# Kernel tuning notes

Hardware: AMD Instinct MI355X
Metric: run time of the kernel (lower is better)

The kernel has to match this reference:

```python
import jax, jax.numpy as jnp
import numpy as np

B = 512
D_MODEL = 512
D_STATE = 128
D_CONV = 2
EXPAND = 2
D_INNER = EXPAND * D_MODEL          # 1024
DT_RANK = (D_MODEL + 15) // 16      # 32 (mamba default 'auto')
HIDDEN = 256


def setup_inputs() -> dict:
    key = jax.random.key(0)
    ks = jax.random.split(key, 12)
    s = 0.02
    f32 = jnp.float32
    inp = {
        "x": jax.random.normal(ks[0], (B, D_MODEL), f32),
        # Mamba params (torch Linear weight layout: [out, in])
        "in_proj_w": jax.random.normal(ks[1], (2 * D_INNER, D_MODEL), f32) * s,
        "conv_w": jax.random.normal(ks[2], (D_INNER, D_CONV), f32) * s,  # depthwise kernel
        "conv_b": jnp.zeros((D_INNER,), f32),
        "x_proj_w": jax.random.normal(ks[3], (DT_RANK + 2 * D_STATE, D_INNER), f32) * s,
        "dt_proj_w": jax.random.normal(ks[4], (D_INNER, DT_RANK), f32) * s,
        "dt_proj_b": jax.random.normal(ks[5], (D_INNER,), f32) * s,
        "A_log": jnp.log(jnp.broadcast_to(
            jnp.arange(1, D_STATE + 1, dtype=f32), (D_INNER, D_STATE)).copy()),
        "D": jnp.ones((D_INNER,), f32),
        "out_proj_w": jax.random.normal(ks[6], (D_MODEL, D_INNER), f32) * s,
        # head params
        "fc1_w": jax.random.normal(ks[7], (HIDDEN, D_MODEL), f32) * s,
        "fc1_b": jnp.zeros((HIDDEN,), f32),
        "fc5_w": jax.random.normal(ks[8], (1, HIDDEN), f32) * s,
        "fc5_b": jnp.zeros((1,), f32),
    }
    return inp


def _mamba(x3, in_proj_w, conv_w, conv_b, x_proj_w, dt_proj_w, dt_proj_b,
           A_log, D, out_proj_w):
    # x3: [B, L, d_model]
    Bn, L, _ = x3.shape
    xz = jnp.einsum('bld,ed->ble', x3, in_proj_w)          # [B, L, 2*d_inner]
    xin, z = xz[..., :D_INNER], xz[..., D_INNER:]
    # depthwise causal conv1d (kernel D_CONV, padding D_CONV-1, truncated to L)
    xp = jnp.pad(xin, ((0, 0), (D_CONV - 1, 0), (0, 0)))
    conv = conv_b
    for k in range(D_CONV):
        conv = conv + conv_w[:, k] * xp[:, k:k + L, :]
    xin = jax.nn.silu(conv)                                 # [B, L, d_inner]
    x_dbl = jnp.einsum('blc,ec->ble', xin, x_proj_w)        # [B, L, dt_rank+2*d_state]
    dt = x_dbl[..., :DT_RANK]
    Bm = x_dbl[..., DT_RANK:DT_RANK + D_STATE]              # [B, L, d_state]
    Cm = x_dbl[..., DT_RANK + D_STATE:]                     # [B, L, d_state]
    dt = jax.nn.softplus(jnp.einsum('blr,cr->blc', dt, dt_proj_w) + dt_proj_b)
    A = -jnp.exp(A_log)                                     # [d_inner, d_state]
    dA = jnp.exp(dt[..., None] * A)                         # [B, L, d_inner, d_state]
    dBu = dt[..., None] * Bm[:, :, None, :] * xin[..., None]

    def step(h, t):
        dA_t, dBu_t, C_t = t
        h = dA_t * h + dBu_t                                # [B, d_inner, d_state]
        y_t = jnp.einsum('bcs,bs->bc', h, C_t)
        return h, y_t

    h0 = jnp.zeros((Bn, D_INNER, D_STATE), x3.dtype)
    _, ys = jax.lax.scan(step, h0, (dA.transpose(1, 0, 2, 3),
                                    dBu.transpose(1, 0, 2, 3),
                                    Cm.transpose(1, 0, 2)))
    y = ys.transpose(1, 0, 2)                               # [B, L, d_inner]
    y = (y + D * xin) * jax.nn.silu(z)
    return jnp.einsum('blc,dc->bld', y, out_proj_w)         # [B, L, d_model]


def reference(x, in_proj_w, conv_w, conv_b, x_proj_w, dt_proj_w, dt_proj_b,
              A_log, D, out_proj_w, fc1_w, fc1_b, fc5_w, fc5_b):
    h = _mamba(x[:, None, :], in_proj_w, conv_w, conv_b, x_proj_w,
               dt_proj_w, dt_proj_b, A_log, D, out_proj_w)[:, 0, :]
    h = h @ fc1_w.T + fc1_b
    h = jnp.where(h >= 0, h, 0.1 * h)   # LeakyReLU(0.1); dropout is eval-mode identity
    h = h @ fc5_w.T + fc5_b
    return jax.nn.sigmoid(h)            # [B, 1]
```

## Files before the change

### kernel.cpp

```cpp
#include <hip/hip_runtime.h>
#include <hip/hip_bf16.h>
#include <cstddef>

typedef __attribute__((ext_vector_type(8))) short short8;
typedef __attribute__((ext_vector_type(4))) float f32x4;

#define MFMA16(a, b, c) __builtin_amdgcn_mfma_f32_16x16x32_bf16((a), (b), (c), 0, 0, 0)

__device__ __forceinline__ unsigned short f2bf(float f) {
    unsigned int u = __float_as_uint(f);
    u = (u + 0x7FFFu + ((u >> 16) & 1u)) >> 16;
    return (unsigned short)u;
}
__device__ __forceinline__ float bf2f(unsigned short h) {
    return __uint_as_float(((unsigned int)h) << 16);
}
__device__ __forceinline__ float silu_f(float v) { return v / (1.f + expf(-v)); }

enum : size_t {
    O_X    = 0,
    O_WIP  = O_X    + 512 * 512,
    O_WXP  = O_WIP  + 2048 * 512,
    O_WDT  = O_WXP  + 288 * 1024,
    O_WOUT = O_WDT  + 1024 * 32,
    O_WFC1 = O_WOUT + 512 * 1024,
    O_XIN  = O_WFC1 + 256 * 512,
    O_SZ   = O_XIN  + 512 * 1024,
    O_XDBL = O_SZ   + 512 * 1024,
    O_Y    = O_XDBL + 512 * 288,
    O_MOUT = O_Y    + 512 * 1024,
};

__device__ __forceinline__ void cvt_seg(const float* __restrict__ s,
                                        unsigned short* __restrict__ d,
                                        int n, int tid, int np)
{
    for (int i = tid * 4; i < n; i += np * 4) {
        float4 v = *reinterpret_cast<const float4*>(s + i);
        ushort4 o;
        o.x = f2bf(v.x); o.y = f2bf(v.y); o.z = f2bf(v.z); o.w = f2bf(v.w);
        *reinterpret_cast<ushort4*>(d + i) = o;
    }
}

__global__ __launch_bounds__(256) void k_convert(
    const float* __restrict__ x,    const float* __restrict__ wip,
    const float* __restrict__ wxp,  const float* __restrict__ wdt,
    const float* __restrict__ wout, const float* __restrict__ wfc1,
    unsigned short* __restrict__ dst)
{
    const int tid = blockIdx.x * blockDim.x + threadIdx.x;
    const int np  = gridDim.x * blockDim.x;
    cvt_seg(x,    dst + O_X,    512 * 512,   tid, np);
    cvt_seg(wip,  dst + O_WIP,  2048 * 512,  tid, np);
    cvt_seg(wxp,  dst + O_WXP,  288 * 1024,  tid, np);
    cvt_seg(wdt,  dst + O_WDT,  1024 * 32,   tid, np);
    cvt_seg(wout, dst + O_WOUT, 512 * 1024,  tid, np);
    cvt_seg(wfc1, dst + O_WFC1, 256 * 512,   tid, np);
}

__global__ __launch_bounds__(256, 2) void k_s1(
    unsigned short* __restrict__ wsb,
    const float* __restrict__ cw, const float* __restrict__ cb)
{
    const int tid = threadIdx.x;
    const int w = tid >> 6, lane = tid & 63, l15 = lane & 15, g = lane >> 4;
    const int n0 = blockIdx.x * 64;
    const int m0 = blockIdx.y * 64 + w * 16;

    const unsigned short* ab = wsb + O_X   + (size_t)(m0 + l15) * 512 + g * 8;
    const unsigned short* bb = wsb + O_WIP + (size_t)(n0 + l15) * 512 + g * 8;

    f32x4 acc[4] = {};
#pragma unroll 4
    for (int k0 = 0; k0 < 512; k0 += 32) {
        short8 a = *reinterpret_cast<const short8*>(ab + k0);
#pragma unroll
        for (int f = 0; f < 4; ++f) {
            short8 b = *reinterpret_cast<const short8*>(bb + f * 16 * 512 + k0);
            acc[f] = MFMA16(a, b, acc[f]);
        }
    }

    const bool xhalf = (n0 < 1024);
    unsigned short* dst = wsb + (xhalf ? O_XIN : O_SZ);
#pragma unroll
    for (int f = 0; f < 4; ++f) {
        int n = n0 + f * 16 + l15;
        int c = xhalf ? n : n - 1024;
        float cwv = 0.f, cbv = 0.f;
        if (xhalf) { cwv = cw[2 * n + 1]; cbv = cb[n]; }
#pragma unroll
        for (int i = 0; i < 4; ++i) {
            int r = m0 + g * 4 + i;
            float v = acc[f][i];
            v = xhalf ? silu_f(cbv + cwv * v) : silu_f(v);
            dst[(size_t)r * 1024 + c] = f2bf(v);
        }
    }
}

__global__ __launch_bounds__(256, 2) void k_s2(unsigned short* __restrict__ wsb)
{
    const int tid = threadIdx.x;
    const int w = tid >> 6, lane = tid & 63, l15 = lane & 15, g = lane >> 4;
    const int n0 = blockIdx.x * 16;
    const int m0 = blockIdx.y * 64 + w * 16;

    const unsigned short* ab = wsb + O_XIN + (size_t)(m0 + l15) * 1024 + g * 8;
    const unsigned short* bb = wsb + O_WXP + (size_t)(n0 + l15) * 1024 + g * 8;

    f32x4 acc = {};
#pragma unroll 4
    for (int k0 = 0; k0 < 1024; k0 += 32) {
        short8 a = *reinterpret_cast<const short8*>(ab + k0);
        short8 b = *reinterpret_cast<const short8*>(bb + k0);
        acc = MFMA16(a, b, acc);
    }
    unsigned short* xd = wsb + O_XDBL;
#pragma unroll
    for (int i = 0; i < 4; ++i)
        xd[(size_t)(m0 + g * 4 + i) * 288 + n0 + l15] = f2bf(acc[i]);
}

__global__ __launch_bounds__(256, 2) void k_s3(
    unsigned short* __restrict__ wsb,
    const float* __restrict__ dtb, const float* __restrict__ Dv)
{
    __shared__ float bcp[16][17];
    __shared__ float bc_s[16];
    const int tid = threadIdx.x;
    const int w = tid >> 6, lane = tid & 63, l15 = lane & 15, g = lane >> 4;
    const int n0 = blockIdx.x * 256;
    const int m0 = blockIdx.y * 16;

    const unsigned short* xd = wsb + O_XDBL;
    {
        int r = tid >> 4, p = tid & 15;
        const unsigned short* row = xd + (size_t)(m0 + r) * 288;
        float s = 0.f;
#pragma unroll
        for (int q = 0; q < 16; ++q)
            s += bf2f(row[32 + p * 16 + q]) * bf2f(row[160 + p * 16 + q]);
        bcp[r][p] = s;
    }
    short8 a = *reinterpret_cast<const short8*>(xd + (size_t)(m0 + l15) * 288 + g * 8);
    __syncthreads();
    if (tid < 16) {
        float s = 0.f;
#pragma unroll
        for (int p = 0; p < 16; ++p) s += bcp[tid][p];
        bc_s[tid] = s;
    }
    __syncthreads();

    const unsigned short* wdt  = wsb + O_WDT;
    const unsigned short* xinb = wsb + O_XIN;
    const unsigned short* szb  = wsb + O_SZ;
    unsigned short* yb = wsb + O_Y;
    const f32x4 z4 = {0.f, 0.f, 0.f, 0.f};
#pragma unroll
    for (int f = 0; f < 4; ++f) {
        int n = n0 + w * 64 + f * 16 + l15;
        short8 b = *reinterpret_cast<const short8*>(wdt + (size_t)n * 32 + g * 8);
        f32x4 acc = MFMA16(a, b, z4);
        float dtbv = dtb[n], Dvv = Dv[n];
#pragma unroll
        for (int i = 0; i < 4; ++i) {
            int r = m0 + g * 4 + i;
            float dtv = acc[i] + dtbv;
            dtv = (dtv > 20.f) ? dtv : log1pf(expf(dtv));
            float yv = bf2f(xinb[(size_t)r * 1024 + n]) *
                       (dtv * bc_s[g * 4 + i] + Dvv) *
                       bf2f(szb[(size_t)r * 1024 + n]);
            yb[(size_t)r * 1024 + n] = f2bf(yv);
        }
    }
}

__global__ __launch_bounds__(256, 2) void k_s4(unsigned short* __restrict__ wsb)
{
    const int tid = threadIdx.x;
    const int w = tid >> 6, lane = tid & 63, l15 = lane & 15, g = lane >> 4;
    const int n0 = blockIdx.x * 64;
    const int m0 = blockIdx.y * 64 + w * 16;

    const unsigned short* ab = wsb + O_Y    + (size_t)(m0 + l15) * 1024 + g * 8;
    const unsigned short* bb = wsb + O_WOUT + (size_t)(n0 + l15) * 1024 + g * 8;

    f32x4 acc[4] = {};
#pragma unroll 4
    for (int k0 = 0; k0 < 1024; k0 += 32) {
        short8 a = *reinterpret_cast<const short8*>(ab + k0);
#pragma unroll
        for (int f = 0; f < 4; ++f) {
            short8 b = *reinterpret_cast<const short8*>(bb + f * 16 * 1024 + k0);
            acc[f] = MFMA16(a, b, acc[f]);
        }
    }
    unsigned short* mo = wsb + O_MOUT;
#pragma unroll
    for (int f = 0; f < 4; ++f)
#pragma unroll
        for (int i = 0; i < 4; ++i)
            mo[(size_t)(m0 + g * 4 + i) * 512 + n0 + f * 16 + l15] = f2bf(acc[f][i]);
}

__global__ __launch_bounds__(256, 2) void k_s5(
    unsigned short* __restrict__ wsb,
    const float* __restrict__ bfc1, const float* __restrict__ wfc5,
    const float* __restrict__ bfc5, float* __restrict__ out)
{
    __shared__ float red[16][72];
    const int tid = threadIdx.x;
    const int w = tid >> 6, lane = tid & 63, l15 = lane & 15, g = lane >> 4;
    const int m0 = blockIdx.x * 16;

    const unsigned short* ab = wsb + O_MOUT + (size_t)(m0 + l15) * 512 + g * 8;
    const unsigned short* bb = wsb + O_WFC1 + (size_t)(w * 64 + l15) * 512 + g * 8;

    f32x4 acc[4] = {};
#pragma unroll 4
    for (int k0 = 0; k0 < 512; k0 += 32) {
        short8 a = *reinterpret_cast<const short8*>(ab + k0);
#pragma unroll
        for (int f = 0; f < 4; ++f) {
            short8 b = *reinterpret_cast<const short8*>(bb + f * 16 * 512 + k0);
            acc[f] = MFMA16(a, b, acc[f]);
        }
    }
    float part[4] = {0.f, 0.f, 0.f, 0.f};
#pragma unroll
    for (int f = 0; f < 4; ++f) {
        int n = w * 64 + f * 16 + l15;
        float b1 = bfc1[n], w5 = wfc5[n];
#pragma unroll
        for (int i = 0; i < 4; ++i) {
            float v = acc[f][i] + b1;
            v = v >= 0.f ? v : 0.1f * v;
            part[i] = fmaf(v, w5, part[i]);
        }
    }
#pragma unroll
    for (int i = 0; i < 4; ++i) red[g * 4 + i][w * 16 + l15] = part[i];
    __syncthreads();
    if (tid < 16) {
        float s = 0.f;
        for (int j = 0; j < 64; ++j) s += red[tid][j];
        out[m0 + tid] = 1.f / (1.f + expf(-(s + bfc5[0])));
    }
}

extern "C" void kernel_launch(void* const* d_in, const int* in_sizes, int n_in,
                              void* d_out, int out_size, void* d_ws, size_t ws_size,
                              hipStream_t stream)
{
    const float* x    = (const float*)d_in[0];
    const float* wip  = (const float*)d_in[1];
    const float* cw   = (const float*)d_in[2];
    const float* cb   = (const float*)d_in[3];
    const float* wxp  = (const float*)d_in[4];
    const float* wdt  = (const float*)d_in[5];
    const float* bdt  = (const float*)d_in[6];
    const float* Dv   = (const float*)d_in[8];
    const float* wout = (const float*)d_in[9];
    const float* wfc1 = (const float*)d_in[10];
    const float* bfc1 = (const float*)d_in[11];
    const float* wfc5 = (const float*)d_in[12];
    const float* bfc5 = (const float*)d_in[13];
    float* out = (float*)d_out;

    unsigned short* wsb = (unsigned short*)d_ws;

    k_convert<<<dim3(512),   256, 0, stream>>>(x, wip, wxp, wdt, wout, wfc1, wsb);
    k_s1     <<<dim3(32, 8), 256, 0, stream>>>(wsb, cw, cb);
    k_s2     <<<dim3(18, 8), 256, 0, stream>>>(wsb);
    k_s3     <<<dim3(4, 32), 256, 0, stream>>>(wsb, bdt, Dv);
    k_s4     <<<dim3(8, 8),  256, 0, stream>>>(wsb);
    k_s5     <<<dim3(32),    256, 0, stream>>>(wsb, bfc1, wfc5, bfc5, out);
}
```

Before: 157.1 us.

## Fuse all stages into one persistent kernel with atomic grid barriers

Replaces the six separate launches (convert, in_proj, x_proj, dt/y, out_proj, head) with a single persistent kernel of 256 blocks. The stages are separated by a software grid barrier built on an agent-scope atomic counter, which is reset by a memset before launch. The out_proj stage is retiled so each of the 256 blocks does work, and the B·C dot product now sums over 128 state elements instead of 256. This removes per-launch overhead and the idle gaps between dependent kernels. In exchange it relies on all 256 blocks being resident at once, and it adds a barrier spin cost at every stage boundary.

```diff
diff --git a/kernel.cpp b/kernel.cpp
--- a/kernel.cpp
+++ b/kernel.cpp
@@ -6,16 +6,17 @@
 typedef __attribute__((ext_vector_type(4))) float f32x4;
 
 #define MFMA16(a, b, c) __builtin_amdgcn_mfma_f32_16x16x32_bf16((a), (b), (c), 0, 0, 0)
-
-__device__ __forceinline__ unsigned short f2bf(float f) {
+#define NBLK 256
+
+static __device__ __forceinline__ unsigned short f2bf(float f) {
     unsigned int u = __float_as_uint(f);
     u = (u + 0x7FFFu + ((u >> 16) & 1u)) >> 16;
     return (unsigned short)u;
 }
-__device__ __forceinline__ float bf2f(unsigned short h) {
+static __device__ __forceinline__ float bf2f(unsigned short h) {
     return __uint_as_float(((unsigned int)h) << 16);
 }
-__device__ __forceinline__ float silu_f(float v) { return v / (1.f + expf(-v)); }
+static __device__ __forceinline__ float silu_f(float v) { return v / (1.f + expf(-v)); }
 
 enum : size_t {
     O_X    = 0,
@@ -29,13 +30,14 @@
     O_XDBL = O_SZ   + 512 * 1024,
     O_Y    = O_XDBL + 512 * 288,
     O_MOUT = O_Y    + 512 * 1024,
+    O_END  = O_MOUT + 512 * 512,
 };
 
-__device__ __forceinline__ void cvt_seg(const float* __restrict__ s,
-                                        unsigned short* __restrict__ d,
-                                        int n, int tid, int np)
-{
-    for (int i = tid * 4; i < n; i += np * 4) {
+static __device__ __forceinline__ void cvt_seg(const float* __restrict__ s,
+                                               unsigned short* __restrict__ d,
+                                               int n, int gt, int np)
+{
+    for (int i = gt * 4; i < n; i += np * 4) {
         float4 v = *reinterpret_cast<const float4*>(s + i);
         ushort4 o;
         o.x = f2bf(v.x); o.y = f2bf(v.y); o.z = f2bf(v.z); o.w = f2bf(v.w);
@@ -43,211 +45,207 @@
     }
 }
 
-__global__ __launch_bounds__(256) void k_convert(
+static __device__ __forceinline__ void grid_barrier(unsigned* cnt, unsigned target)
+{
+    __syncthreads();
+    if (threadIdx.x == 0) {
+        __hip_atomic_fetch_add(cnt, 1u, __ATOMIC_RELEASE, __HIP_MEMORY_SCOPE_AGENT);
+        while (__hip_atomic_load(cnt, __ATOMIC_ACQUIRE, __HIP_MEMORY_SCOPE_AGENT) < target)
+            __builtin_amdgcn_s_sleep(2);
+    }
+    __syncthreads();
+}
+
+__global__ __launch_bounds__(256, 2) void k_net(
     const float* __restrict__ x,    const float* __restrict__ wip,
     const float* __restrict__ wxp,  const float* __restrict__ wdt,
     const float* __restrict__ wout, const float* __restrict__ wfc1,
-    unsigned short* __restrict__ dst)
-{
-    const int tid = blockIdx.x * blockDim.x + threadIdx.x;
-    const int np  = gridDim.x * blockDim.x;
-    cvt_seg(x,    dst + O_X,    512 * 512,   tid, np);
-    cvt_seg(wip,  dst + O_WIP,  2048 * 512,  tid, np);
-    cvt_seg(wxp,  dst + O_WXP,  288 * 1024,  tid, np);
-    cvt_seg(wdt,  dst + O_WDT,  1024 * 32,   tid, np);
-    cvt_seg(wout, dst + O_WOUT, 512 * 1024,  tid, np);
-    cvt_seg(wfc1, dst + O_WFC1, 256 * 512,   tid, np);
-}
-
-__global__ __launch_bounds__(256, 2) void k_s1(
-    unsigned short* __restrict__ wsb,
-    const float* __restrict__ cw, const float* __restrict__ cb)
-{
-    const int tid = threadIdx.x;
-    const int w = tid >> 6, lane = tid & 63, l15 = lane & 15, g = lane >> 4;
-    const int n0 = blockIdx.x * 64;
-    const int m0 = blockIdx.y * 64 + w * 16;
-
-    const unsigned short* ab = wsb + O_X   + (size_t)(m0 + l15) * 512 + g * 8;
-    const unsigned short* bb = wsb + O_WIP + (size_t)(n0 + l15) * 512 + g * 8;
-
-    f32x4 acc[4] = {};
-#pragma unroll 4
-    for (int k0 = 0; k0 < 512; k0 += 32) {
-        short8 a = *reinterpret_cast<const short8*>(ab + k0);
+    const float* __restrict__ cw,   const float* __restrict__ cb,
+    const float* __restrict__ dtb,  const float* __restrict__ Dv,
+    const float* __restrict__ bfc1, const float* __restrict__ wfc5,
+    const float* __restrict__ bfc5,
+    unsigned short* __restrict__ wsb, unsigned* __restrict__ bar,
+    float* __restrict__ out)
+{
+    __shared__ float smem[16 * 72];
+    const int tid  = threadIdx.x;
+    const int bid  = blockIdx.x;
+    const int w    = tid >> 6;
+    const int lane = tid & 63;
+    const int l15  = lane & 15;
+    const int g    = lane >> 4;
+
+    {
+        const int gt = bid * 256 + tid, np = NBLK * 256;
+        cvt_seg(x,    wsb + O_X,    512 * 512,  gt, np);
+        cvt_seg(wip,  wsb + O_WIP,  2048 * 512, gt, np);
+        cvt_seg(wxp,  wsb + O_WXP,  288 * 1024, gt, np);
+        cvt_seg(wdt,  wsb + O_WDT,  1024 * 32,  gt, np);
+        cvt_seg(wout, wsb + O_WOUT, 512 * 1024, gt, np);
+        cvt_seg(wfc1, wsb + O_WFC1, 256 * 512,  gt, np);
+    }
+    grid_barrier(bar, NBLK * 1);
+
+    {
+        const int n0 = (bid & 31) * 64;
+        const int m0 = (bid >> 5) * 64 + w * 16;
+        const unsigned short* ab = wsb + O_X   + (size_t)(m0 + l15) * 512 + g * 8;
+        const unsigned short* bb = wsb + O_WIP + (size_t)(n0 + l15) * 512 + g * 8;
+        f32x4 acc[4] = {};
+#pragma unroll 4
+        for (int k0 = 0; k0 < 512; k0 += 32) {
+            short8 a = *reinterpret_cast<const short8*>(ab + k0);
+#pragma unroll
+            for (int f = 0; f < 4; ++f) {
+                short8 b = *reinterpret_cast<const short8*>(bb + f * 16 * 512 + k0);
+                acc[f] = MFMA16(a, b, acc[f]);
+            }
+        }
+        const bool xhalf = (n0 < 1024);
+        unsigned short* dst = wsb + (xhalf ? O_XIN : O_SZ);
 #pragma unroll
         for (int f = 0; f < 4; ++f) {
-            short8 b = *reinterpret_cast<const short8*>(bb + f * 16 * 512 + k0);
-            acc[f] = MFMA16(a, b, acc[f]);
-        }
-    }
-
-    const bool xhalf = (n0 < 1024);
-    unsigned short* dst = wsb + (xhalf ? O_XIN : O_SZ);
-#pragma unroll
-    for (int f = 0; f < 4; ++f) {
-        int n = n0 + f * 16 + l15;
-        int c = xhalf ? n : n - 1024;
-        float cwv = 0.f, cbv = 0.f;
-        if (xhalf) { cwv = cw[2 * n + 1]; cbv = cb[n]; }
-#pragma unroll
-        for (int i = 0; i < 4; ++i) {
-            int r = m0 + g * 4 + i;
-            float v = acc[f][i];
-            v = xhalf ? silu_f(cbv + cwv * v) : silu_f(v);
-            dst[(size_t)r * 1024 + c] = f2bf(v);
-        }
-    }
-}
-
-__global__ __launch_bounds__(256, 2) void k_s2(unsigned short* __restrict__ wsb)
-{
-    const int tid = threadIdx.x;
-    const int w = tid >> 6, lane = tid & 63, l15 = lane & 15, g = lane >> 4;
-    const int n0 = blockIdx.x * 16;
-    const int m0 = blockIdx.y * 64 + w * 16;
-
-    const unsigned short* ab = wsb + O_XIN + (size_t)(m0 + l15) * 1024 + g * 8;
-    const unsigned short* bb = wsb + O_WXP + (size_t)(n0 + l15) * 1024 + g * 8;
-
-    f32x4 acc = {};
-#pragma unroll 4
-    for (int k0 = 0; k0 < 1024; k0 += 32) {
-        short8 a = *reinterpret_cast<const short8*>(ab + k0);
-        short8 b = *reinterpret_cast<const short8*>(bb + k0);
-        acc = MFMA16(a, b, acc);
-    }
-    unsigned short* xd = wsb + O_XDBL;
-#pragma unroll
-    for (int i = 0; i < 4; ++i)
-        xd[(size_t)(m0 + g * 4 + i) * 288 + n0 + l15] = f2bf(acc[i]);
-}
-
-__global__ __launch_bounds__(256, 2) void k_s3(
-    unsigned short* __restrict__ wsb,
-    const float* __restrict__ dtb, const float* __restrict__ Dv)
-{
-    __shared__ float bcp[16][17];
-    __shared__ float bc_s[16];
-    const int tid = threadIdx.x;
-    const int w = tid >> 6, lane = tid & 63, l15 = lane & 15, g = lane >> 4;
-    const int n0 = blockIdx.x * 256;
-    const int m0 = blockIdx.y * 16;
-
-    const unsigned short* xd = wsb + O_XDBL;
-    {
-        int r = tid >> 4, p = tid & 15;
-        const unsigned short* row = xd + (size_t)(m0 + r) * 288;
-        float s = 0.f;
-#pragma unroll
-        for (int q = 0; q < 16; ++q)
-            s += bf2f(row[32 + p * 16 + q]) * bf2f(row[160 + p * 16 + q]);
-        bcp[r][p] = s;
-    }
-    short8 a = *reinterpret_cast<const short8*>(xd + (size_t)(m0 + l15) * 288 + g * 8);
-    __syncthreads();
-    if (tid < 16) {
-        float s = 0.f;
-#pragma unroll
-        for (int p = 0; p < 16; ++p) s += bcp[tid][p];
-        bc_s[tid] = s;
-    }
-    __syncthreads();
-
-    const unsigned short* wdt  = wsb + O_WDT;
-    const unsigned short* xinb = wsb + O_XIN;
-    const unsigned short* szb  = wsb + O_SZ;
-    unsigned short* yb = wsb + O_Y;
-    const f32x4 z4 = {0.f, 0.f, 0.f, 0.f};
-#pragma unroll
-    for (int f = 0; f < 4; ++f) {
-        int n = n0 + w * 64 + f * 16 + l15;
-        short8 b = *reinterpret_cast<const short8*>(wdt + (size_t)n * 32 + g * 8);
-        f32x4 acc = MFMA16(a, b, z4);
-        float dtbv = dtb[n], Dvv = Dv[n];
-#pragma unroll
-        for (int i = 0; i < 4; ++i) {
-            int r = m0 + g * 4 + i;
-            float dtv = acc[i] + dtbv;
-            dtv = (dtv > 20.f) ? dtv : log1pf(expf(dtv));
-            float yv = bf2f(xinb[(size_t)r * 1024 + n]) *
-                       (dtv * bc_s[g * 4 + i] + Dvv) *
-                       bf2f(szb[(size_t)r * 1024 + n]);
-            yb[(size_t)r * 1024 + n] = f2bf(yv);
-        }
-    }
-}
-
-__global__ __launch_bounds__(256, 2) void k_s4(unsigned short* __restrict__ wsb)
-{
-    const int tid = threadIdx.x;
-    const int w = tid >> 6, lane = tid & 63, l15 = lane & 15, g = lane >> 4;
-    const int n0 = blockIdx.x * 64;
-    const int m0 = blockIdx.y * 64 + w * 16;
-
-    const unsigned short* ab = wsb + O_Y    + (size_t)(m0 + l15) * 1024 + g * 8;
-    const unsigned short* bb = wsb + O_WOUT + (size_t)(n0 + l15) * 1024 + g * 8;
-
-    f32x4 acc[4] = {};
-#pragma unroll 4
-    for (int k0 = 0; k0 < 1024; k0 += 32) {
-        short8 a = *reinterpret_cast<const short8*>(ab + k0);
+            int n = n0 + f * 16 + l15;
+            int c = xhalf ? n : n - 1024;
+            float cwv = 0.f, cbv = 0.f;
+            if (xhalf) { cwv = cw[2 * n + 1]; cbv = cb[n]; }
+#pragma unroll
+            for (int i = 0; i < 4; ++i) {
+                int r = m0 + g * 4 + i;
+                float v = acc[f][i];
+                v = xhalf ? silu_f(cbv + cwv * v) : silu_f(v);
+                dst[(size_t)r * 1024 + c] = f2bf(v);
+            }
+        }
+    }
+    grid_barrier(bar, NBLK * 2);
+
+    {
+        const int u = bid * 4 + w;
+        if (u < 576) {
+            const int n0 = (u % 18) * 16;
+            const int m0 = (u / 18) * 16;
+            const unsigned short* ab = wsb + O_XIN + (size_t)(m0 + l15) * 1024 + g * 8;
+            const unsigned short* bb = wsb + O_WXP + (size_t)(n0 + l15) * 1024 + g * 8;
+            f32x4 acc = {};
+#pragma unroll 4
+            for (int k0 = 0; k0 < 1024; k0 += 32) {
+                short8 a = *reinterpret_cast<const short8*>(ab + k0);
+                short8 b = *reinterpret_cast<const short8*>(bb + k0);
+                acc = MFMA16(a, b, acc);
+            }
+            unsigned short* xd = wsb + O_XDBL;
+#pragma unroll
+            for (int i = 0; i < 4; ++i)
+                xd[(size_t)(m0 + g * 4 + i) * 288 + n0 + l15] = f2bf(acc[i]);
+        }
+    }
+    grid_barrier(bar, NBLK * 3);
+
+    if (bid < 128) {
+        const int m0 = (bid >> 2) * 16;
+        const int n0 = (bid & 3) * 256;
+        const unsigned short* xd = wsb + O_XDBL;
+        float* bcp  = smem;
+        float* bc_s = smem + 16 * 17;
+        {
+            int r = tid >> 4, p = tid & 15;
+            const unsigned short* row = xd + (size_t)(m0 + r) * 288;
+            float s = 0.f;
+#pragma unroll
+            for (int q = 0; q < 8; ++q)
+                s += bf2f(row[32 + p * 8 + q]) * bf2f(row[160 + p * 8 + q]);
+            bcp[r * 17 + p] = s;
+        }
+        short8 a = *reinterpret_cast<const short8*>(xd + (size_t)(m0 + l15) * 288 + g * 8);
+        __syncthreads();
+        if (tid < 16) {
+            float s = 0.f;
+#pragma unroll
+            for (int p = 0; p < 16; ++p) s += bcp[tid * 17 + p];
+            bc_s[tid] = s;
+        }
+        __syncthreads();
+
+        const unsigned short* wdtb = wsb + O_WDT;
+        const unsigned short* xinb = wsb + O_XIN;
+        const unsigned short* szb  = wsb + O_SZ;
+        unsigned short* yb = wsb + O_Y;
+        const f32x4 z4 = {0.f, 0.f, 0.f, 0.f};
 #pragma unroll
         for (int f = 0; f < 4; ++f) {
-            short8 b = *reinterpret_cast<const short8*>(bb + f * 16 * 1024 + k0);
-            acc[f] = MFMA16(a, b, acc[f]);
-        }
-    }
-    unsigned short* mo = wsb + O_MOUT;
-#pragma unroll
-    for (int f = 0; f < 4; ++f)
+            int n = n0 + w * 64 + f * 16 + l15;
+            short8 b = *reinterpret_cast<const short8*>(wdtb + (size_t)n * 32 + g * 8);
+            f32x4 acc = MFMA16(a, b, z4);
+            float dtbv = dtb[n], Dvv = Dv[n];
+#pragma unroll
+            for (int i = 0; i < 4; ++i) {
+                int r = m0 + g * 4 + i;
+                float dtv = acc[i] + dtbv;
+                dtv = (dtv > 20.f) ? dtv : log1pf(expf(dtv));
+                float yv = bf2f(xinb[(size_t)r * 1024 + n]) *
+                           (dtv * bc_s[g * 4 + i] + Dvv) *
+                           bf2f(szb[(size_t)r * 1024 + n]);
+                yb[(size_t)r * 1024 + n] = f2bf(yv);
+            }
+        }
+    }
+    grid_barrier(bar, NBLK * 4);
+
+    {
+        const int n0 = (bid & 7) * 64 + w * 16;
+        const int m0 = (bid >> 3) * 16;
+        const unsigned short* ab = wsb + O_Y    + (size_t)(m0 + l15) * 1024 + g * 8;
+        const unsigned short* bb = wsb + O_WOUT + (size_t)(n0 + l15) * 1024 + g * 8;
+        f32x4 acc = {};
+#pragma unroll 4
+        for (int k0 = 0; k0 < 1024; k0 += 32) {
+            short8 a = *reinterpret_cast<const short8*>(ab + k0);
+            short8 b = *reinterpret_cast<const short8*>(bb + k0);
+            acc = MFMA16(a, b, acc);
+        }
+        unsigned short* mo = wsb + O_MOUT;
 #pragma unroll
         for (int i = 0; i < 4; ++i)
-            mo[(size_t)(m0 + g * 4 + i) * 512 + n0 + f * 16 + l15] = f2bf(acc[f][i]);
-}
-
-__global__ __launch_bounds__(256, 2) void k_s5(
-    unsigned short* __restrict__ wsb,
-    const float* __restrict__ bfc1, const float* __restrict__ wfc5,
-    const float* __restrict__ bfc5, float* __restrict__ out)
-{
-    __shared__ float red[16][72];
-    const int tid = threadIdx.x;
-    const int w = tid >> 6, lane = tid & 63, l15 = lane & 15, g = lane >> 4;
-    const int m0 = blockIdx.x * 16;
-
-    const unsigned short* ab = wsb + O_MOUT + (size_t)(m0 + l15) * 512 + g * 8;
-    const unsigned short* bb = wsb + O_WFC1 + (size_t)(w * 64 + l15) * 512 + g * 8;
-
-    f32x4 acc[4] = {};
-#pragma unroll 4
-    for (int k0 = 0; k0 < 512; k0 += 32) {
-        short8 a = *reinterpret_cast<const short8*>(ab + k0);
+            mo[(size_t)(m0 + g * 4 + i) * 512 + n0 + l15] = f2bf(acc[i]);
+    }
+    grid_barrier(bar, NBLK * 5);
+
+    if (bid < 32) {
+        const int m0 = bid * 16;
+        const unsigned short* ab = wsb + O_MOUT + (size_t)(m0 + l15) * 512 + g * 8;
+        const unsigned short* bb = wsb + O_WFC1 + (size_t)(w * 64 + l15) * 512 + g * 8;
+        f32x4 acc[4] = {};
+#pragma unroll 4
+        for (int k0 = 0; k0 < 512; k0 += 32) {
+            short8 a = *reinterpret_cast<const short8*>(ab + k0);
+#pragma unroll
+            for (int f = 0; f < 4; ++f) {
+                short8 b = *reinterpret_cast<const short8*>(bb + f * 16 * 512 + k0);
+                acc[f] = MFMA16(a, b, acc[f]);
+            }
+        }
+        float part[4] = {0.f, 0.f, 0.f, 0.f};
 #pragma unroll
         for (int f = 0; f < 4; ++f) {
-            short8 b = *reinterpret_cast<const short8*>(bb + f * 16 * 512 + k0);
-            acc[f] = MFMA16(a, b, acc[f]);
-        }
-    }
-    float part[4] = {0.f, 0.f, 0.f, 0.f};
-#pragma unroll
-    for (int f = 0; f < 4; ++f) {
-        int n = w * 64 + f * 16 + l15;
-        float b1 = bfc1[n], w5 = wfc5[n];
-#pragma unroll
-        for (int i = 0; i < 4; ++i) {
-            float v = acc[f][i] + b1;
-            v = v >= 0.f ? v : 0.1f * v;
-            part[i] = fmaf(v, w5, part[i]);
-        }
-    }
-#pragma unroll
-    for (int i = 0; i < 4; ++i) red[g * 4 + i][w * 16 + l15] = part[i];
-    __syncthreads();
-    if (tid < 16) {
-        float s = 0.f;
-        for (int j = 0; j < 64; ++j) s += red[tid][j];
-        out[m0 + tid] = 1.f / (1.f + expf(-(s + bfc5[0])));
+            int n = w * 64 + f * 16 + l15;
+            float b1 = bfc1[n], w5 = wfc5[n];
+#pragma unroll
+            for (int i = 0; i < 4; ++i) {
+                float v = acc[f][i] + b1;
+                v = v >= 0.f ? v : 0.1f * v;
+                part[i] = fmaf(v, w5, part[i]);
+            }
+        }
+        float* red = smem;
+#pragma unroll
+        for (int i = 0; i < 4; ++i) red[(g * 4 + i) * 72 + w * 16 + l15] = part[i];
+        __syncthreads();
+        if (tid < 16) {
+            float s = 0.f;
+            for (int j = 0; j < 64; ++j) s += red[tid * 72 + j];
+            out[m0 + tid] = 1.f / (1.f + expf(-(s + bfc5[0])));
+        }
     }
 }
 
@@ -271,11 +269,10 @@
     float* out = (float*)d_out;
 
     unsigned short* wsb = (unsigned short*)d_ws;
-
-    k_convert<<<dim3(512),   256, 0, stream>>>(x, wip, wxp, wdt, wout, wfc1, wsb);
-    k_s1     <<<dim3(32, 8), 256, 0, stream>>>(wsb, cw, cb);
-    k_s2     <<<dim3(18, 8), 256, 0, stream>>>(wsb);
-    k_s3     <<<dim3(4, 32), 256, 0, stream>>>(wsb, bdt, Dv);
-    k_s4     <<<dim3(8, 8),  256, 0, stream>>>(wsb);
-    k_s5     <<<dim3(32),    256, 0, stream>>>(wsb, bfc1, wfc5, bfc5, out);
-}
+    unsigned* bar = (unsigned*)(wsb + O_END);
+
+    hipMemsetAsync(bar, 0, 64, stream);
+    k_net<<<NBLK, 256, 0, stream>>>(x, wip, wxp, wdt, wout, wfc1,
+                                    cw, cb, bdt, Dv, bfc1, wfc5, bfc5,
+                                    wsb, bar, out);
+}
```

Result: slower. 239.7 us (+52.5%).
